# Performance work log

Measured on AMD Instinct MI355X. Metric: run time of the kernel, lower is better.

Reference implementation:

```python
import jax, jax.numpy as jnp
import numpy as np
from jax import lax

B, T, D, K = 512, 512, 64, 1024
COMMITMENT_LOSS_FACTOR = 0.1
QUANTIZATION_LOSS_FACTOR = 0.2


def setup_inputs() -> dict:
    key = jax.random.key(0)
    k1, k2 = jax.random.split(key)
    h = jax.random.normal(k1, (B, T, D), dtype=jnp.float32)
    # codebook init: uniform(-1/K, 1/K), matching nn.Embedding init in the module
    weight = jax.random.uniform(k2, (K, D), dtype=jnp.float32, minval=-1.0 / K, maxval=1.0 / K)
    return {"h": h, "weight": weight}


def reference(h, weight):
    d = weight.shape[1]
    hf = h.reshape(-1, d)                                   # [N, D]
    # squared euclidean distances via expanded norms + matmul  -> [N, K]
    dist = ((hf ** 2).sum(-1, keepdims=True)
            + (weight ** 2).sum(-1)
            - 2.0 * hf @ weight.T)
    closest = jnp.argmin(dist, axis=-1)                     # [N]
    quantized_indices = closest[:, None]                    # [N, 1]
    # one_hot @ weight is exactly a row gather
    quantized = jnp.take(weight, closest, axis=0)           # [N, D]
    commitment_loss = ((lax.stop_gradient(quantized) - hf) ** 2).mean(-1)  # [N]
    embedding_loss = ((quantized - lax.stop_gradient(hf)) ** 2).mean(-1)   # [N]
    # straight-through estimator
    quantized_st = (hf + lax.stop_gradient(quantized - hf)).reshape(h.shape)
    loss = (commitment_loss * COMMITMENT_LOSS_FACTOR
            + embedding_loss * QUANTIZATION_LOSS_FACTOR)    # [N]
    return quantized_st, quantized_indices, loss
```

## Files before the change

kernel.cpp:

```cpp
#include <hip/hip_runtime.h>
#include <math.h>

#define NROWS (512 * 512)
#define KCB   1024
#define DDIM  64
#define NQ    ((size_t)NROWS * DDIM)
#define RPW   32
#define CMAX  8
#define WAVES 16
#define BLKT  1024
#define NBLK  256
#define ITERS 2

typedef __attribute__((ext_vector_type(8))) short bf16x8;
typedef __attribute__((ext_vector_type(4))) float f32x4;

__device__ __forceinline__ unsigned short f2bf(float x) {
    unsigned u = __float_as_uint(x);
    u = u + 0x7FFFu + ((u >> 16) & 1u);
    return (unsigned short)(u >> 16);
}
__device__ __forceinline__ unsigned fsort(float d) {
    unsigned u = __float_as_uint(d);
    return (u & 0x80000000u) ? ~u : (u | 0x80000000u);
}

__global__ __launch_bounds__(1024)
void prep_w(const float* __restrict__ w, float* __restrict__ bsq,
            unsigned short* __restrict__ wbf, float* __restrict__ wmaxp) {
    __shared__ float red[16];
    const int k = threadIdx.x;
    const float* row = w + (size_t)k * DDIM;
    float r[8];
#pragma unroll
    for (int j = 0; j < 8; ++j) r[j] = __fmul_rn(row[j], row[j]);
#pragma unroll
    for (int i = 8; i < DDIM; i += 8)
#pragma unroll
        for (int j = 0; j < 8; ++j)
            r[j] = __fadd_rn(r[j], __fmul_rn(row[i + j], row[i + j]));
    float b = __fadd_rn(__fadd_rn(__fadd_rn(r[0], r[1]), __fadd_rn(r[2], r[3])),
                        __fadd_rn(__fadd_rn(r[4], r[5]), __fadd_rn(r[6], r[7])));
    bsq[k] = b;
    unsigned* dst = (unsigned*)(wbf + (size_t)k * DDIM);
#pragma unroll
    for (int j = 0; j < 32; ++j)
        dst[j] = (unsigned)f2bf(row[2 * j]) | ((unsigned)f2bf(row[2 * j + 1]) << 16);
    float v = sqrtf(b) * 1.02f;
#pragma unroll
    for (int off = 1; off < 64; off <<= 1) v = fmaxf(v, __shfl_xor(v, off));
    if ((threadIdx.x & 63) == 0) red[threadIdx.x >> 6] = v;
    __syncthreads();
    if (threadIdx.x == 0) {
        float m = red[0];
#pragma unroll
        for (int j = 1; j < 16; ++j) m = fmaxf(m, red[j]);
        *wmaxp = m;
    }
}

__global__ __launch_bounds__(BLKT, 1)
void vq_scan(const float* __restrict__ h, const float* __restrict__ w,
             const unsigned short* __restrict__ wbf, const float* __restrict__ bsq,
             const float* __restrict__ wmaxp, float* __restrict__ out) {
    __shared__ float4 s4[KCB * 8];
    __shared__ float smb[KCB];
    __shared__ int scnt[WAVES][RPW];
    __shared__ unsigned short sclist[WAVES][RPW][CMAX];
    __shared__ unsigned long long sbkey[WAVES][RPW];

    const int tid = threadIdx.x;
    const int wv = tid >> 6, lane = tid & 63;
    const int l16 = lane & 15, lh = lane >> 4;

    {
        const float4* g4 = reinterpret_cast<const float4*>(wbf);
#pragma unroll
        for (int j = 0; j < 8; ++j) {
            int F = j * BLKT + tid;
            int r = F >> 3, c = F & 7;
            s4[F] = g4[r * 8 + (c ^ (r & 7))];
        }
        smb[tid] = __fmul_rn(bsq[tid], -0.5f);
    }
    __syncthreads();

    const int sw = l16 & 7;
    const int C0 = lh ^ sw;
    const int C1 = (4 + lh) ^ sw;
    const float wmaxv = *wmaxp;

#pragma unroll 1
    for (int it = 0; it < ITERS; ++it) {
        const size_t rowbase = ((size_t)blockIdx.x * WAVES + wv) * (RPW * ITERS) + (size_t)it * RPW;

        if (lane < RPW) { scnt[wv][lane] = 0; sbkey[wv][lane] = 0xFFFFFFFFFFFFFFFFULL; }

        float af = 0.f;
        if (lane < RPW) {
            const float* row = h + (size_t)(rowbase + lane) * DDIM;
            float hr[DDIM];
#pragma unroll
            for (int i = 0; i < DDIM; i += 4) {
                float4 v = *reinterpret_cast<const float4*>(row + i);
                hr[i] = v.x; hr[i + 1] = v.y; hr[i + 2] = v.z; hr[i + 3] = v.w;
            }
            float s[8];
#pragma unroll
            for (int j = 0; j < 8; ++j) s[j] = __fmul_rn(hr[j], hr[j]);
#pragma unroll
            for (int i = 8; i < DDIM; i += 8)
#pragma unroll
                for (int j = 0; j < 8; ++j)
                    s[j] = __fadd_rn(s[j], __fmul_rn(hr[i + j], hr[i + j]));
            af = __fadd_rn(__fadd_rn(__fadd_rn(s[0], s[1]), __fadd_rn(s[2], s[3])),
                           __fadd_rn(__fadd_rn(s[4], s[5]), __fadd_rn(s[6], s[7])));
        }

        bf16x8 afr[2][2];
#pragma unroll
        for (int mt = 0; mt < 2; ++mt) {
            const float* hrow = h + ((size_t)(rowbase + mt * 16 + l16)) * DDIM;
#pragma unroll
            for (int dh = 0; dh < 2; ++dh) {
                float4 a = *reinterpret_cast<const float4*>(hrow + dh * 32 + lh * 8);
                float4 bq = *reinterpret_cast<const float4*>(hrow + dh * 32 + lh * 8 + 4);
                union { bf16x8 v; unsigned short u[8]; } pk;
                pk.u[0] = f2bf(a.x); pk.u[1] = f2bf(a.y); pk.u[2] = f2bf(a.z); pk.u[3] = f2bf(a.w);
                pk.u[4] = f2bf(bq.x); pk.u[5] = f2bf(bq.y); pk.u[6] = f2bf(bq.z); pk.u[7] = f2bf(bq.w);
                afr[mt][dh] = pk.v;
            }
        }

        float pmax[8];
#pragma unroll
        for (int j = 0; j < 8; ++j) pmax[j] = -INFINITY;

#pragma unroll 1
        for (int ch = 0; ch < 8; ++ch) {
            float4 cb0[8], cb1[8];
            float cmb[8];
#pragma unroll
            for (int t = 0; t < 8; ++t) {
                const int lr = (ch * 8 + t) * 16 + l16;
                cb0[t] = s4[lr * 8 + C0];
                cb1[t] = s4[lr * 8 + C1];
                cmb[t] = smb[lr];
            }
#pragma unroll
            for (int t = 0; t < 8; ++t) {
                bf16x8 bfr0 = *reinterpret_cast<const bf16x8*>(&cb0[t]);
                bf16x8 bfr1 = *reinterpret_cast<const bf16x8*>(&cb1[t]);
                f32x4 acc0 = {cmb[t], cmb[t], cmb[t], cmb[t]};
#pragma unroll
                for (int mt = 0; mt < 2; ++mt) {
                    f32x4 acc = acc0;
                    acc = __builtin_amdgcn_mfma_f32_16x16x32_bf16(afr[mt][0], bfr0, acc, 0, 0, 0);
                    acc = __builtin_amdgcn_mfma_f32_16x16x32_bf16(afr[mt][1], bfr1, acc, 0, 0, 0);
#pragma unroll
                    for (int i = 0; i < 4; ++i)
                        pmax[mt * 4 + i] = fmaxf(pmax[mt * 4 + i], acc[i]);
                }
            }
        }

#pragma unroll
        for (int off = 1; off < 16; off <<= 1)
#pragma unroll
            for (int j = 0; j < 8; ++j) pmax[j] = fmaxf(pmax[j], __shfl_xor(pmax[j], off));
        float trA[8];
#pragma unroll
        for (int mt = 0; mt < 2; ++mt)
#pragma unroll
            for (int i = 0; i < 4; ++i) {
                float Afr = __shfl(af, mt * 16 + lh * 4 + i);
                trA[mt * 4 + i] = pmax[mt * 4 + i]
                                - (sqrtf(Afr) * 1.001f * wmaxv * 0.015625f + 5e-4f);
            }

#pragma unroll 1
        for (int ch = 0; ch < 8; ++ch) {
            float4 cb0[8], cb1[8];
            float cmb[8];
#pragma unroll
            for (int t = 0; t < 8; ++t) {
                const int lr = (ch * 8 + t) * 16 + l16;
                cb0[t] = s4[lr * 8 + C0];
                cb1[t] = s4[lr * 8 + C1];
                cmb[t] = smb[lr];
            }
#pragma unroll
            for (int t = 0; t < 8; ++t) {
                bf16x8 bfr0 = *reinterpret_cast<const bf16x8*>(&cb0[t]);
                bf16x8 bfr1 = *reinterpret_cast<const bf16x8*>(&cb1[t]);
                f32x4 acc0 = {cmb[t], cmb[t], cmb[t], cmb[t]};
                const int kk = (ch * 8 + t) * 16 + l16;
#pragma unroll
                for (int mt = 0; mt < 2; ++mt) {
                    f32x4 acc = acc0;
                    acc = __builtin_amdgcn_mfma_f32_16x16x32_bf16(afr[mt][0], bfr0, acc, 0, 0, 0);
                    acc = __builtin_amdgcn_mfma_f32_16x16x32_bf16(afr[mt][1], bfr1, acc, 0, 0, 0);
#pragma unroll
                    for (int i = 0; i < 4; ++i) {
                        if (acc[i] >= trA[mt * 4 + i]) {
                            int row = mt * 16 + lh * 4 + i;
                            int slot = atomicAdd(&scnt[wv][row], 1);
                            if (slot < CMAX) sclist[wv][row][slot] = (unsigned short)kk;
                        }
                    }
                }
            }
        }
        __builtin_amdgcn_wave_barrier();

        {
            const int row = lane >> 1;
            const int s0 = lane & 1;
            const float Afr = __shfl(af, row);
            const int cnt = scnt[wv][row];
            if (cnt <= CMAX && s0 < cnt) {
                const size_t ng = rowbase + row;
                const float* hrow = h + ng * DDIM;
                float hreg[DDIM];
#pragma unroll
                for (int i = 0; i < DDIM; i += 4) {
                    float4 v = *reinterpret_cast<const float4*>(hrow + i);
                    hreg[i] = v.x; hreg[i + 1] = v.y; hreg[i + 2] = v.z; hreg[i + 3] = v.w;
                }
                for (int slot = s0; slot < cnt; slot += 2) {
                    int k = sclist[wv][row][slot];
                    const float* wr = w + (size_t)k * DDIM;
                    float acc = 0.f;
#pragma unroll
                    for (int i = 0; i < DDIM; i += 4) {
                        float4 x = *reinterpret_cast<const float4*>(wr + i);
                        acc = fmaf(hreg[i + 0], x.x, acc);
                        acc = fmaf(hreg[i + 1], x.y, acc);
                        acc = fmaf(hreg[i + 2], x.z, acc);
                        acc = fmaf(hreg[i + 3], x.w, acc);
                    }
                    float d = __fsub_rn(__fadd_rn(Afr, bsq[k]), __fadd_rn(acc, acc));
                    unsigned long long key = ((unsigned long long)fsort(d) << 32) | (unsigned)k;
                    atomicMin(&sbkey[wv][row], key);
                }
            }
        }
#pragma unroll 1
        for (int r = 0; r < RPW; ++r) {
            const float Afr = __shfl(af, r);
            if (scnt[wv][r] > CMAX) {
                const size_t ng = rowbase + r;
                const float* hrow = h + ng * DDIM;
                float hreg[DDIM];
#pragma unroll
                for (int i = 0; i < DDIM; i += 4) {
                    float4 v = *reinterpret_cast<const float4*>(hrow + i);
                    hreg[i] = v.x; hreg[i + 1] = v.y; hreg[i + 2] = v.z; hreg[i + 3] = v.w;
                }
                for (int k = lane; k < KCB; k += 64) {
                    const float* wr = w + (size_t)k * DDIM;
                    float acc = 0.f;
#pragma unroll
                    for (int i = 0; i < DDIM; i += 4) {
                        float4 x = *reinterpret_cast<const float4*>(wr + i);
                        acc = fmaf(hreg[i + 0], x.x, acc);
                        acc = fmaf(hreg[i + 1], x.y, acc);
                        acc = fmaf(hreg[i + 2], x.z, acc);
                        acc = fmaf(hreg[i + 3], x.w, acc);
                    }
                    float d = __fsub_rn(__fadd_rn(Afr, bsq[k]), __fadd_rn(acc, acc));
                    unsigned long long key = ((unsigned long long)fsort(d) << 32) | (unsigned)k;
                    atomicMin(&sbkey[wv][r], key);
                }
            }
        }
        __builtin_amdgcn_wave_barrier();

        if (lane < RPW)
            out[NQ + rowbase + lane] = (float)(unsigned)(sbkey[wv][lane] & 0xFFFFFFFFu);

#pragma unroll
        for (int q = 0; q < 8; ++q) {
            const int idx = q * 64 + lane;
            const int row = idx >> 4, c4 = idx & 15;
            const int bk = (int)(unsigned)(sbkey[wv][row] & 0xFFFFFFFFu);
            const size_t ng = rowbase + row;
            float4 hq = *reinterpret_cast<const float4*>(h + ng * DDIM + 4 * c4);
            float4 wq = *reinterpret_cast<const float4*>(w + (size_t)bk * DDIM + 4 * c4);
            float4 o;
            o.x = __fadd_rn(hq.x, __fsub_rn(wq.x, hq.x));
            o.y = __fadd_rn(hq.y, __fsub_rn(wq.y, hq.y));
            o.z = __fadd_rn(hq.z, __fsub_rn(wq.z, hq.z));
            o.w = __fadd_rn(hq.w, __fsub_rn(wq.w, hq.w));
            *reinterpret_cast<float4*>(out + ng * DDIM + 4 * c4) = o;
        }

        if (lane < RPW) {
            const int bk = (int)(unsigned)(sbkey[wv][lane] & 0xFFFFFFFFu);
            const size_t ng = rowbase + lane;
            const float* hrow = h + ng * DDIM;
            const float* qrow = w + (size_t)bk * DDIM;
            float hr[DDIM];
#pragma unroll
            for (int i = 0; i < DDIM; i += 4) {
                float4 v = *reinterpret_cast<const float4*>(hrow + i);
                hr[i] = v.x; hr[i + 1] = v.y; hr[i + 2] = v.z; hr[i + 3] = v.w;
            }
            float r2[8];
#pragma unroll
            for (int c = 0; c < 8; ++c) {
                float4 qa = *reinterpret_cast<const float4*>(qrow + 8 * c);
                float4 qb = *reinterpret_cast<const float4*>(qrow + 8 * c + 4);
                float d0 = __fsub_rn(qa.x, hr[8 * c + 0]);
                float d1 = __fsub_rn(qa.y, hr[8 * c + 1]);
                float d2 = __fsub_rn(qa.z, hr[8 * c + 2]);
                float d3 = __fsub_rn(qa.w, hr[8 * c + 3]);
                float d4 = __fsub_rn(qb.x, hr[8 * c + 4]);
                float d5 = __fsub_rn(qb.y, hr[8 * c + 5]);
                float d6 = __fsub_rn(qb.z, hr[8 * c + 6]);
                float d7 = __fsub_rn(qb.w, hr[8 * c + 7]);
                if (c == 0) {
                    r2[0] = __fmul_rn(d0, d0); r2[1] = __fmul_rn(d1, d1);
                    r2[2] = __fmul_rn(d2, d2); r2[3] = __fmul_rn(d3, d3);
                    r2[4] = __fmul_rn(d4, d4); r2[5] = __fmul_rn(d5, d5);
                    r2[6] = __fmul_rn(d6, d6); r2[7] = __fmul_rn(d7, d7);
                } else {
                    r2[0] = __fadd_rn(r2[0], __fmul_rn(d0, d0));
                    r2[1] = __fadd_rn(r2[1], __fmul_rn(d1, d1));
                    r2[2] = __fadd_rn(r2[2], __fmul_rn(d2, d2));
                    r2[3] = __fadd_rn(r2[3], __fmul_rn(d3, d3));
                    r2[4] = __fadd_rn(r2[4], __fmul_rn(d4, d4));
                    r2[5] = __fadd_rn(r2[5], __fmul_rn(d5, d5));
                    r2[6] = __fadd_rn(r2[6], __fmul_rn(d6, d6));
                    r2[7] = __fadd_rn(r2[7], __fmul_rn(d7, d7));
                }
            }
            float S = __fadd_rn(__fadd_rn(__fadd_rn(r2[0], r2[1]), __fadd_rn(r2[2], r2[3])),
                                __fadd_rn(__fadd_rn(r2[4], r2[5]), __fadd_rn(r2[6], r2[7])));
            float m = __fmul_rn(S, 0.015625f);
            out[NQ + NROWS + ng] = __fadd_rn(__fmul_rn(m, 0.1f), __fmul_rn(m, 0.2f));
        }
    }
}

extern "C" void kernel_launch(void* const* d_in, const int* in_sizes, int n_in,
                              void* d_out, int out_size, void* d_ws, size_t ws_size,
                              hipStream_t stream) {
    (void)in_sizes; (void)n_in; (void)out_size; (void)ws_size;
    const float* h = (const float*)d_in[0];
    const float* w = (const float*)d_in[1];
    float* out = (float*)d_out;

    char* ws = (char*)d_ws;
    float* bsq = (float*)ws;
    float* wmaxp = (float*)(ws + 4096);
    unsigned short* wbf = (unsigned short*)(ws + 8192);

    prep_w<<<1, 1024, 0, stream>>>(w, bsq, wbf, wmaxp);
    vq_scan<<<NBLK, BLKT, 0, stream>>>(h, w, wbf, bsq, wmaxp, out);
}
```

Measured before the change: 265.1 us.

## Process 64 rows per wave in one pass and use per-lane candidate refinement

Each wave now handles 64 rows in a single pass with four MFMA row tiles, so every shared-memory codebook fragment load feeds twice as many MFMAs and the outer iteration loop is gone. Candidate refinement is now one lane per row doing a sequential argmin in registers, replacing two-lanes-per-row 64-bit atomicMin keys. The fallback path uses a wave shuffle reduction instead of shared atomics. This raises register pressure (16 pmax/trA values, 8 A fragments) and lowers CMAX to 6, so more rows may fall into the slow full-scan path.

After: 612.4 us. 2.31x slower.

```diff
diff --git a/kernel.cpp b/kernel.cpp
--- a/kernel.cpp
+++ b/kernel.cpp
@@ -5,12 +5,11 @@
 #define KCB   1024
 #define DDIM  64
 #define NQ    ((size_t)NROWS * DDIM)
-#define RPW   32
-#define CMAX  8
+#define RPW   64
+#define CMAX  6
 #define WAVES 16
 #define BLKT  1024
 #define NBLK  256
-#define ITERS 2
 
 typedef __attribute__((ext_vector_type(8))) short bf16x8;
 typedef __attribute__((ext_vector_type(4))) float f32x4;
@@ -19,10 +18,6 @@
     unsigned u = __float_as_uint(x);
     u = u + 0x7FFFu + ((u >> 16) & 1u);
     return (unsigned short)(u >> 16);
-}
-__device__ __forceinline__ unsigned fsort(float d) {
-    unsigned u = __float_as_uint(d);
-    return (u & 0x80000000u) ? ~u : (u | 0x80000000u);
 }
 
 __global__ __launch_bounds__(1024)
@@ -67,11 +62,12 @@
     __shared__ float smb[KCB];
     __shared__ int scnt[WAVES][RPW];
     __shared__ unsigned short sclist[WAVES][RPW][CMAX];
-    __shared__ unsigned long long sbkey[WAVES][RPW];
+    __shared__ unsigned int sbk[WAVES][RPW];
 
     const int tid = threadIdx.x;
     const int wv = tid >> 6, lane = tid & 63;
     const int l16 = lane & 15, lh = lane >> 4;
+    const size_t rowbase = ((size_t)blockIdx.x * WAVES + wv) * RPW;
 
     {
         const float4* g4 = reinterpret_cast<const float4*>(wbf);
@@ -83,6 +79,7 @@
         }
         smb[tid] = __fmul_rn(bsq[tid], -0.5f);
     }
+    scnt[wv][lane] = 0;
     __syncthreads();
 
     const int sw = l16 & 7;
@@ -90,256 +87,257 @@
     const int C1 = (4 + lh) ^ sw;
     const float wmaxv = *wmaxp;
 
+    float af;
+    {
+        const float* row = h + (size_t)(rowbase + lane) * DDIM;
+        float hr[DDIM];
+#pragma unroll
+        for (int i = 0; i < DDIM; i += 4) {
+            float4 v = *reinterpret_cast<const float4*>(row + i);
+            hr[i] = v.x; hr[i + 1] = v.y; hr[i + 2] = v.z; hr[i + 3] = v.w;
+        }
+        float s[8];
+#pragma unroll
+        for (int j = 0; j < 8; ++j) s[j] = __fmul_rn(hr[j], hr[j]);
+#pragma unroll
+        for (int i = 8; i < DDIM; i += 8)
+#pragma unroll
+            for (int j = 0; j < 8; ++j)
+                s[j] = __fadd_rn(s[j], __fmul_rn(hr[i + j], hr[i + j]));
+        af = __fadd_rn(__fadd_rn(__fadd_rn(s[0], s[1]), __fadd_rn(s[2], s[3])),
+                       __fadd_rn(__fadd_rn(s[4], s[5]), __fadd_rn(s[6], s[7])));
+    }
+
+    bf16x8 afr[4][2];
+#pragma unroll
+    for (int mt = 0; mt < 4; ++mt) {
+        const float* hrow = h + ((size_t)(rowbase + mt * 16 + l16)) * DDIM;
+#pragma unroll
+        for (int dh = 0; dh < 2; ++dh) {
+            float4 a = *reinterpret_cast<const float4*>(hrow + dh * 32 + lh * 8);
+            float4 bq = *reinterpret_cast<const float4*>(hrow + dh * 32 + lh * 8 + 4);
+            union { bf16x8 v; unsigned short u[8]; } pk;
+            pk.u[0] = f2bf(a.x); pk.u[1] = f2bf(a.y); pk.u[2] = f2bf(a.z); pk.u[3] = f2bf(a.w);
+            pk.u[4] = f2bf(bq.x); pk.u[5] = f2bf(bq.y); pk.u[6] = f2bf(bq.z); pk.u[7] = f2bf(bq.w);
+            afr[mt][dh] = pk.v;
+        }
+    }
+
+    float pmax[16];
+#pragma unroll
+    for (int j = 0; j < 16; ++j) pmax[j] = -INFINITY;
+
 #pragma unroll 1
-    for (int it = 0; it < ITERS; ++it) {
-        const size_t rowbase = ((size_t)blockIdx.x * WAVES + wv) * (RPW * ITERS) + (size_t)it * RPW;
-
-        if (lane < RPW) { scnt[wv][lane] = 0; sbkey[wv][lane] = 0xFFFFFFFFFFFFFFFFULL; }
-
-        float af = 0.f;
-        if (lane < RPW) {
-            const float* row = h + (size_t)(rowbase + lane) * DDIM;
-            float hr[DDIM];
-#pragma unroll
-            for (int i = 0; i < DDIM; i += 4) {
-                float4 v = *reinterpret_cast<const float4*>(row + i);
-                hr[i] = v.x; hr[i + 1] = v.y; hr[i + 2] = v.z; hr[i + 3] = v.w;
-            }
-            float s[8];
-#pragma unroll
-            for (int j = 0; j < 8; ++j) s[j] = __fmul_rn(hr[j], hr[j]);
-#pragma unroll
-            for (int i = 8; i < DDIM; i += 8)
-#pragma unroll
-                for (int j = 0; j < 8; ++j)
-                    s[j] = __fadd_rn(s[j], __fmul_rn(hr[i + j], hr[i + j]));
-            af = __fadd_rn(__fadd_rn(__fadd_rn(s[0], s[1]), __fadd_rn(s[2], s[3])),
-                           __fadd_rn(__fadd_rn(s[4], s[5]), __fadd_rn(s[6], s[7])));
-        }
-
-        bf16x8 afr[2][2];
-#pragma unroll
-        for (int mt = 0; mt < 2; ++mt) {
-            const float* hrow = h + ((size_t)(rowbase + mt * 16 + l16)) * DDIM;
-#pragma unroll
-            for (int dh = 0; dh < 2; ++dh) {
-                float4 a = *reinterpret_cast<const float4*>(hrow + dh * 32 + lh * 8);
-                float4 bq = *reinterpret_cast<const float4*>(hrow + dh * 32 + lh * 8 + 4);
-                union { bf16x8 v; unsigned short u[8]; } pk;
-                pk.u[0] = f2bf(a.x); pk.u[1] = f2bf(a.y); pk.u[2] = f2bf(a.z); pk.u[3] = f2bf(a.w);
-                pk.u[4] = f2bf(bq.x); pk.u[5] = f2bf(bq.y); pk.u[6] = f2bf(bq.z); pk.u[7] = f2bf(bq.w);
-                afr[mt][dh] = pk.v;
-            }
-        }
-
-        float pmax[8];
-#pragma unroll
-        for (int j = 0; j < 8; ++j) pmax[j] = -INFINITY;
+    for (int ch = 0; ch < 8; ++ch) {
+        float4 cb0[8], cb1[8];
+        float cmb[8];
+#pragma unroll
+        for (int t = 0; t < 8; ++t) {
+            const int lr = (ch * 8 + t) * 16 + l16;
+            cb0[t] = s4[lr * 8 + C0];
+            cb1[t] = s4[lr * 8 + C1];
+            cmb[t] = smb[lr];
+        }
+#pragma unroll
+        for (int t = 0; t < 8; ++t) {
+            bf16x8 bfr0 = *reinterpret_cast<const bf16x8*>(&cb0[t]);
+            bf16x8 bfr1 = *reinterpret_cast<const bf16x8*>(&cb1[t]);
+            f32x4 acc0 = {cmb[t], cmb[t], cmb[t], cmb[t]};
+#pragma unroll
+            for (int mt = 0; mt < 4; ++mt) {
+                f32x4 acc = acc0;
+                acc = __builtin_amdgcn_mfma_f32_16x16x32_bf16(afr[mt][0], bfr0, acc, 0, 0, 0);
+                acc = __builtin_amdgcn_mfma_f32_16x16x32_bf16(afr[mt][1], bfr1, acc, 0, 0, 0);
+#pragma unroll
+                for (int i = 0; i < 4; ++i)
+                    pmax[mt * 4 + i] = fmaxf(pmax[mt * 4 + i], acc[i]);
+            }
+        }
+    }
+
+#pragma unroll
+    for (int off = 1; off < 16; off <<= 1)
+#pragma unroll
+        for (int j = 0; j < 16; ++j) pmax[j] = fmaxf(pmax[j], __shfl_xor(pmax[j], off));
+    float trA[16];
+#pragma unroll
+    for (int mt = 0; mt < 4; ++mt)
+#pragma unroll
+        for (int i = 0; i < 4; ++i) {
+            float Afr = __shfl(af, mt * 16 + lh * 4 + i);
+            trA[mt * 4 + i] = pmax[mt * 4 + i]
+                            - (sqrtf(Afr) * 1.001f * wmaxv * 0.015625f + 5e-4f);
+        }
 
 #pragma unroll 1
-        for (int ch = 0; ch < 8; ++ch) {
-            float4 cb0[8], cb1[8];
-            float cmb[8];
-#pragma unroll
-            for (int t = 0; t < 8; ++t) {
-                const int lr = (ch * 8 + t) * 16 + l16;
-                cb0[t] = s4[lr * 8 + C0];
-                cb1[t] = s4[lr * 8 + C1];
-                cmb[t] = smb[lr];
-            }
-#pragma unroll
-            for (int t = 0; t < 8; ++t) {
-                bf16x8 bfr0 = *reinterpret_cast<const bf16x8*>(&cb0[t]);
-                bf16x8 bfr1 = *reinterpret_cast<const bf16x8*>(&cb1[t]);
-                f32x4 acc0 = {cmb[t], cmb[t], cmb[t], cmb[t]};
-#pragma unroll
-                for (int mt = 0; mt < 2; ++mt) {
-                    f32x4 acc = acc0;
-                    acc = __builtin_amdgcn_mfma_f32_16x16x32_bf16(afr[mt][0], bfr0, acc, 0, 0, 0);
-                    acc = __builtin_amdgcn_mfma_f32_16x16x32_bf16(afr[mt][1], bfr1, acc, 0, 0, 0);
-#pragma unroll
-                    for (int i = 0; i < 4; ++i)
-                        pmax[mt * 4 + i] = fmaxf(pmax[mt * 4 + i], acc[i]);
-                }
-            }
-        }
-
-#pragma unroll
-        for (int off = 1; off < 16; off <<= 1)
-#pragma unroll
-            for (int j = 0; j < 8; ++j) pmax[j] = fmaxf(pmax[j], __shfl_xor(pmax[j], off));
-        float trA[8];
-#pragma unroll
-        for (int mt = 0; mt < 2; ++mt)
-#pragma unroll
-            for (int i = 0; i < 4; ++i) {
-                float Afr = __shfl(af, mt * 16 + lh * 4 + i);
-                trA[mt * 4 + i] = pmax[mt * 4 + i]
-                                - (sqrtf(Afr) * 1.001f * wmaxv * 0.015625f + 5e-4f);
-            }
-
-#pragma unroll 1
-        for (int ch = 0; ch < 8; ++ch) {
-            float4 cb0[8], cb1[8];
-            float cmb[8];
-#pragma unroll
-            for (int t = 0; t < 8; ++t) {
-                const int lr = (ch * 8 + t) * 16 + l16;
-                cb0[t] = s4[lr * 8 + C0];
-                cb1[t] = s4[lr * 8 + C1];
-                cmb[t] = smb[lr];
-            }
-#pragma unroll
-            for (int t = 0; t < 8; ++t) {
-                bf16x8 bfr0 = *reinterpret_cast<const bf16x8*>(&cb0[t]);
-                bf16x8 bfr1 = *reinterpret_cast<const bf16x8*>(&cb1[t]);
-                f32x4 acc0 = {cmb[t], cmb[t], cmb[t], cmb[t]};
-                const int kk = (ch * 8 + t) * 16 + l16;
-#pragma unroll
-                for (int mt = 0; mt < 2; ++mt) {
-                    f32x4 acc = acc0;
-                    acc = __builtin_amdgcn_mfma_f32_16x16x32_bf16(afr[mt][0], bfr0, acc, 0, 0, 0);
-                    acc = __builtin_amdgcn_mfma_f32_16x16x32_bf16(afr[mt][1], bfr1, acc, 0, 0, 0);
-#pragma unroll
-                    for (int i = 0; i < 4; ++i) {
-                        if (acc[i] >= trA[mt * 4 + i]) {
-                            int row = mt * 16 + lh * 4 + i;
-                            int slot = atomicAdd(&scnt[wv][row], 1);
-                            if (slot < CMAX) sclist[wv][row][slot] = (unsigned short)kk;
-                        }
+    for (int ch = 0; ch < 8; ++ch) {
+        float4 cb0[8], cb1[8];
+        float cmb[8];
+#pragma unroll
+        for (int t = 0; t < 8; ++t) {
+            const int lr = (ch * 8 + t) * 16 + l16;
+            cb0[t] = s4[lr * 8 + C0];
+            cb1[t] = s4[lr * 8 + C1];
+            cmb[t] = smb[lr];
+        }
+#pragma unroll
+        for (int t = 0; t < 8; ++t) {
+            bf16x8 bfr0 = *reinterpret_cast<const bf16x8*>(&cb0[t]);
+            bf16x8 bfr1 = *reinterpret_cast<const bf16x8*>(&cb1[t]);
+            f32x4 acc0 = {cmb[t], cmb[t], cmb[t], cmb[t]};
+            const int kk = (ch * 8 + t) * 16 + l16;
+#pragma unroll
+            for (int mt = 0; mt < 4; ++mt) {
+                f32x4 acc = acc0;
+                acc = __builtin_amdgcn_mfma_f32_16x16x32_bf16(afr[mt][0], bfr0, acc, 0, 0, 0);
+                acc = __builtin_amdgcn_mfma_f32_16x16x32_bf16(afr[mt][1], bfr1, acc, 0, 0, 0);
+#pragma unroll
+                for (int i = 0; i < 4; ++i) {
+                    if (acc[i] >= trA[mt * 4 + i]) {
+                        int row = mt * 16 + lh * 4 + i;
+                        int slot = atomicAdd(&scnt[wv][row], 1);
+                        if (slot < CMAX) sclist[wv][row][slot] = (unsigned short)kk;
                     }
                 }
             }
         }
-        __builtin_amdgcn_wave_barrier();
-
-        {
-            const int row = lane >> 1;
-            const int s0 = lane & 1;
-            const float Afr = __shfl(af, row);
-            const int cnt = scnt[wv][row];
-            if (cnt <= CMAX && s0 < cnt) {
-                const size_t ng = rowbase + row;
-                const float* hrow = h + ng * DDIM;
-                float hreg[DDIM];
-#pragma unroll
-                for (int i = 0; i < DDIM; i += 4) {
-                    float4 v = *reinterpret_cast<const float4*>(hrow + i);
-                    hreg[i] = v.x; hreg[i + 1] = v.y; hreg[i + 2] = v.z; hreg[i + 3] = v.w;
-                }
-                for (int slot = s0; slot < cnt; slot += 2) {
-                    int k = sclist[wv][row][slot];
-                    const float* wr = w + (size_t)k * DDIM;
-                    float acc = 0.f;
-#pragma unroll
-                    for (int i = 0; i < DDIM; i += 4) {
-                        float4 x = *reinterpret_cast<const float4*>(wr + i);
-                        acc = fmaf(hreg[i + 0], x.x, acc);
-                        acc = fmaf(hreg[i + 1], x.y, acc);
-                        acc = fmaf(hreg[i + 2], x.z, acc);
-                        acc = fmaf(hreg[i + 3], x.w, acc);
-                    }
-                    float d = __fsub_rn(__fadd_rn(Afr, bsq[k]), __fadd_rn(acc, acc));
-                    unsigned long long key = ((unsigned long long)fsort(d) << 32) | (unsigned)k;
-                    atomicMin(&sbkey[wv][row], key);
-                }
-            }
-        }
-#pragma unroll 1
-        for (int r = 0; r < RPW; ++r) {
-            const float Afr = __shfl(af, r);
-            if (scnt[wv][r] > CMAX) {
-                const size_t ng = rowbase + r;
-                const float* hrow = h + ng * DDIM;
-                float hreg[DDIM];
-#pragma unroll
-                for (int i = 0; i < DDIM; i += 4) {
-                    float4 v = *reinterpret_cast<const float4*>(hrow + i);
-                    hreg[i] = v.x; hreg[i + 1] = v.y; hreg[i + 2] = v.z; hreg[i + 3] = v.w;
-                }
-                for (int k = lane; k < KCB; k += 64) {
-                    const float* wr = w + (size_t)k * DDIM;
-                    float acc = 0.f;
-#pragma unroll
-                    for (int i = 0; i < DDIM; i += 4) {
-                        float4 x = *reinterpret_cast<const float4*>(wr + i);
-                        acc = fmaf(hreg[i + 0], x.x, acc);
-                        acc = fmaf(hreg[i + 1], x.y, acc);
-                        acc = fmaf(hreg[i + 2], x.z, acc);
-                        acc = fmaf(hreg[i + 3], x.w, acc);
-                    }
-                    float d = __fsub_rn(__fadd_rn(Afr, bsq[k]), __fadd_rn(acc, acc));
-                    unsigned long long key = ((unsigned long long)fsort(d) << 32) | (unsigned)k;
-                    atomicMin(&sbkey[wv][r], key);
-                }
-            }
-        }
-        __builtin_amdgcn_wave_barrier();
-
-        if (lane < RPW)
-            out[NQ + rowbase + lane] = (float)(unsigned)(sbkey[wv][lane] & 0xFFFFFFFFu);
-
-#pragma unroll
-        for (int q = 0; q < 8; ++q) {
-            const int idx = q * 64 + lane;
-            const int row = idx >> 4, c4 = idx & 15;
-            const int bk = (int)(unsigned)(sbkey[wv][row] & 0xFFFFFFFFu);
-            const size_t ng = rowbase + row;
-            float4 hq = *reinterpret_cast<const float4*>(h + ng * DDIM + 4 * c4);
-            float4 wq = *reinterpret_cast<const float4*>(w + (size_t)bk * DDIM + 4 * c4);
-            float4 o;
-            o.x = __fadd_rn(hq.x, __fsub_rn(wq.x, hq.x));
-            o.y = __fadd_rn(hq.y, __fsub_rn(wq.y, hq.y));
-            o.z = __fadd_rn(hq.z, __fsub_rn(wq.z, hq.z));
-            o.w = __fadd_rn(hq.w, __fsub_rn(wq.w, hq.w));
-            *reinterpret_cast<float4*>(out + ng * DDIM + 4 * c4) = o;
-        }
-
-        if (lane < RPW) {
-            const int bk = (int)(unsigned)(sbkey[wv][lane] & 0xFFFFFFFFu);
+    }
+    __builtin_amdgcn_wave_barrier();
+
+    {
+        const int cnt = scnt[wv][lane];
+        if (cnt <= CMAX) {
             const size_t ng = rowbase + lane;
             const float* hrow = h + ng * DDIM;
-            const float* qrow = w + (size_t)bk * DDIM;
-            float hr[DDIM];
+            float hreg[DDIM];
 #pragma unroll
             for (int i = 0; i < DDIM; i += 4) {
                 float4 v = *reinterpret_cast<const float4*>(hrow + i);
-                hr[i] = v.x; hr[i + 1] = v.y; hr[i + 2] = v.z; hr[i + 3] = v.w;
-            }
-            float r2[8];
-#pragma unroll
-            for (int c = 0; c < 8; ++c) {
-                float4 qa = *reinterpret_cast<const float4*>(qrow + 8 * c);
-                float4 qb = *reinterpret_cast<const float4*>(qrow + 8 * c + 4);
-                float d0 = __fsub_rn(qa.x, hr[8 * c + 0]);
-                float d1 = __fsub_rn(qa.y, hr[8 * c + 1]);
-                float d2 = __fsub_rn(qa.z, hr[8 * c + 2]);
-                float d3 = __fsub_rn(qa.w, hr[8 * c + 3]);
-                float d4 = __fsub_rn(qb.x, hr[8 * c + 4]);
-                float d5 = __fsub_rn(qb.y, hr[8 * c + 5]);
-                float d6 = __fsub_rn(qb.z, hr[8 * c + 6]);
-                float d7 = __fsub_rn(qb.w, hr[8 * c + 7]);
-                if (c == 0) {
-                    r2[0] = __fmul_rn(d0, d0); r2[1] = __fmul_rn(d1, d1);
-                    r2[2] = __fmul_rn(d2, d2); r2[3] = __fmul_rn(d3, d3);
-                    r2[4] = __fmul_rn(d4, d4); r2[5] = __fmul_rn(d5, d5);
-                    r2[6] = __fmul_rn(d6, d6); r2[7] = __fmul_rn(d7, d7);
-                } else {
-                    r2[0] = __fadd_rn(r2[0], __fmul_rn(d0, d0));
-                    r2[1] = __fadd_rn(r2[1], __fmul_rn(d1, d1));
-                    r2[2] = __fadd_rn(r2[2], __fmul_rn(d2, d2));
-                    r2[3] = __fadd_rn(r2[3], __fmul_rn(d3, d3));
-                    r2[4] = __fadd_rn(r2[4], __fmul_rn(d4, d4));
-                    r2[5] = __fadd_rn(r2[5], __fmul_rn(d5, d5));
-                    r2[6] = __fadd_rn(r2[6], __fmul_rn(d6, d6));
-                    r2[7] = __fadd_rn(r2[7], __fmul_rn(d7, d7));
+                hreg[i] = v.x; hreg[i + 1] = v.y; hreg[i + 2] = v.z; hreg[i + 3] = v.w;
+            }
+            float dbest = INFINITY;
+            int kbest = 0x7FFFFFFF;
+            for (int slot = 0; slot < cnt; ++slot) {
+                int k = sclist[wv][lane][slot];
+                const float* wr = w + (size_t)k * DDIM;
+                float acc = 0.f;
+#pragma unroll
+                for (int i = 0; i < DDIM; i += 4) {
+                    float4 x = *reinterpret_cast<const float4*>(wr + i);
+                    acc = fmaf(hreg[i + 0], x.x, acc);
+                    acc = fmaf(hreg[i + 1], x.y, acc);
+                    acc = fmaf(hreg[i + 2], x.z, acc);
+                    acc = fmaf(hreg[i + 3], x.w, acc);
                 }
-            }
-            float S = __fadd_rn(__fadd_rn(__fadd_rn(r2[0], r2[1]), __fadd_rn(r2[2], r2[3])),
-                                __fadd_rn(__fadd_rn(r2[4], r2[5]), __fadd_rn(r2[6], r2[7])));
-            float m = __fmul_rn(S, 0.015625f);
-            out[NQ + NROWS + ng] = __fadd_rn(__fmul_rn(m, 0.1f), __fmul_rn(m, 0.2f));
-        }
+                float d = __fsub_rn(__fadd_rn(af, bsq[k]), __fadd_rn(acc, acc));
+                if (d < dbest || (d == dbest && k < kbest)) { dbest = d; kbest = k; }
+            }
+            sbk[wv][lane] = (unsigned)kbest;
+        }
+    }
+#pragma unroll 1
+    for (int r = 0; r < RPW; ++r) {
+        if (scnt[wv][r] > CMAX) {
+            const float Afr = __shfl(af, r);
+            const size_t ng = rowbase + r;
+            const float* hrow = h + ng * DDIM;
+            float hreg[DDIM];
+#pragma unroll
+            for (int i = 0; i < DDIM; i += 4) {
+                float4 v = *reinterpret_cast<const float4*>(hrow + i);
+                hreg[i] = v.x; hreg[i + 1] = v.y; hreg[i + 2] = v.z; hreg[i + 3] = v.w;
+            }
+            float dbest = INFINITY;
+            int kbest = 0x7FFFFFFF;
+            for (int k = lane; k < KCB; k += 64) {
+                const float* wr = w + (size_t)k * DDIM;
+                float acc = 0.f;
+#pragma unroll
+                for (int i = 0; i < DDIM; i += 4) {
+                    float4 x = *reinterpret_cast<const float4*>(wr + i);
+                    acc = fmaf(hreg[i + 0], x.x, acc);
+                    acc = fmaf(hreg[i + 1], x.y, acc);
+                    acc = fmaf(hreg[i + 2], x.z, acc);
+                    acc = fmaf(hreg[i + 3], x.w, acc);
+                }
+                float d = __fsub_rn(__fadd_rn(Afr, bsq[k]), __fadd_rn(acc, acc));
+                if (d < dbest || (d == dbest && k < kbest)) { dbest = d; kbest = k; }
+            }
+#pragma unroll
+            for (int off = 1; off < 64; off <<= 1) {
+                float od = __shfl_xor(dbest, off);
+                int ok = __shfl_xor(kbest, off);
+                bool take = (od < dbest) || (od == dbest && ok < kbest);
+                dbest = take ? od : dbest;
+                kbest = take ? ok : kbest;
+            }
+            if (lane == 0) sbk[wv][r] = (unsigned)kbest;
+        }
+    }
+    __builtin_amdgcn_wave_barrier();
+
+    out[NQ + rowbase + lane] = (float)sbk[wv][lane];
+
+#pragma unroll
+    for (int q = 0; q < 16; ++q) {
+        const int idx = q * 64 + lane;
+        const int row = idx >> 4, c4 = idx & 15;
+        const int bk = (int)sbk[wv][row];
+        const size_t ng = rowbase + row;
+        float4 hq = *reinterpret_cast<const float4*>(h + ng * DDIM + 4 * c4);
+        float4 wq = *reinterpret_cast<const float4*>(w + (size_t)bk * DDIM + 4 * c4);
+        float4 o;
+        o.x = __fadd_rn(hq.x, __fsub_rn(wq.x, hq.x));
+        o.y = __fadd_rn(hq.y, __fsub_rn(wq.y, hq.y));
+        o.z = __fadd_rn(hq.z, __fsub_rn(wq.z, hq.z));
+        o.w = __fadd_rn(hq.w, __fsub_rn(wq.w, hq.w));
+        *reinterpret_cast<float4*>(out + ng * DDIM + 4 * c4) = o;
+    }
+
+    {
+        const int bk = (int)sbk[wv][lane];
+        const size_t ng = rowbase + lane;
+        const float* hrow = h + ng * DDIM;
+        const float* qrow = w + (size_t)bk * DDIM;
+        float hr[DDIM];
+#pragma unroll
+        for (int i = 0; i < DDIM; i += 4) {
+            float4 v = *reinterpret_cast<const float4*>(hrow + i);
+            hr[i] = v.x; hr[i + 1] = v.y; hr[i + 2] = v.z; hr[i + 3] = v.w;
+        }
+        float r2[8];
+#pragma unroll
+        for (int c = 0; c < 8; ++c) {
+            float4 qa = *reinterpret_cast<const float4*>(qrow + 8 * c);
+            float4 qb = *reinterpret_cast<const float4*>(qrow + 8 * c + 4);
+            float d0 = __fsub_rn(qa.x, hr[8 * c + 0]);
+            float d1 = __fsub_rn(qa.y, hr[8 * c + 1]);
+            float d2 = __fsub_rn(qa.z, hr[8 * c + 2]);
+            float d3 = __fsub_rn(qa.w, hr[8 * c + 3]);
+            float d4 = __fsub_rn(qb.x, hr[8 * c + 4]);
+            float d5 = __fsub_rn(qb.y, hr[8 * c + 5]);
+            float d6 = __fsub_rn(qb.z, hr[8 * c + 6]);
+            float d7 = __fsub_rn(qb.w, hr[8 * c + 7]);
+            if (c == 0) {
+                r2[0] = __fmul_rn(d0, d0); r2[1] = __fmul_rn(d1, d1);
+                r2[2] = __fmul_rn(d2, d2); r2[3] = __fmul_rn(d3, d3);
+                r2[4] = __fmul_rn(d4, d4); r2[5] = __fmul_rn(d5, d5);
+                r2[6] = __fmul_rn(d6, d6); r2[7] = __fmul_rn(d7, d7);
+            } else {
+                r2[0] = __fadd_rn(r2[0], __fmul_rn(d0, d0));
+                r2[1] = __fadd_rn(r2[1], __fmul_rn(d1, d1));
+                r2[2] = __fadd_rn(r2[2], __fmul_rn(d2, d2));
+                r2[3] = __fadd_rn(r2[3], __fmul_rn(d3, d3));
+                r2[4] = __fadd_rn(r2[4], __fmul_rn(d4, d4));
+                r2[5] = __fadd_rn(r2[5], __fmul_rn(d5, d5));
+                r2[6] = __fadd_rn(r2[6], __fmul_rn(d6, d6));
+                r2[7] = __fadd_rn(r2[7], __fmul_rn(d7, d7));
+            }
+        }
+        float S = __fadd_rn(__fadd_rn(__fadd_rn(r2[0], r2[1]), __fadd_rn(r2[2], r2[3])),
+                            __fadd_rn(__fadd_rn(r2[4], r2[5]), __fadd_rn(r2[6], r2[7])));
+        float m = __fmul_rn(S, 0.015625f);
+        out[NQ + NROWS + ng] = __fadd_rn(__fmul_rn(m, 0.1f), __fmul_rn(m, 0.2f));
     }
 }
 
```
